# Kernel tuning notes

Measured on AMD Instinct MI355X. Metric: run time of the kernel, lower is better.

Reference implementation:

```python
import jax, jax.numpy as jnp
import numpy as np

ALPHA = 0.5  # leak rate (module default)


def setup_inputs() -> dict:
    key = jax.random.key(0)
    k1, k2, k3 = jax.random.split(key, 3)
    T, nInput, nRes = 4096, 4096, 2048
    x = jax.random.normal(k1, (T, nInput), dtype=jnp.float32)
    # gamma=0.01 scaled input weights, as in the module
    Win = 0.01 * jax.random.normal(k2, (nInput, nRes), dtype=jnp.float32)
    # recurrent weights ~ unit spectral radius (1/sqrt(N) scaling of iid gaussian)
    W = jax.random.normal(k3, (nRes, nRes), dtype=jnp.float32) / jnp.sqrt(nRes)
    return {"x": x, "Win": Win, "W": W}


def reference(x, Win, W):
    # Input projection is time-independent -> hoist out of the recurrence.
    uproj = x @ Win  # [T, nRes]

    def step(v, u):
        v_new = (1.0 - ALPHA) * v + ALPHA * jnp.tanh(v @ W + u)
        return v_new, v_new

    v0 = jnp.zeros((W.shape[0],), dtype=x.dtype)
    _, states = jax.lax.scan(step, v0, uproj)  # states: [T, nRes]
    return states
```

## Files before the change

### kernel.cpp

```cpp
#include <hip/hip_runtime.h>

#define NRES 2048
#define NBLK 256
#define RBUF 4

typedef unsigned long long u64;
typedef unsigned int u32;

__global__ __launch_bounds__(256) void transpose_k(const float* __restrict__ W,
                                                   float* __restrict__ Wt) {
  __shared__ float tile[32][33];
  const int tx = threadIdx.x, ty = threadIdx.y;
  const int x = blockIdx.x * 32 + tx;
  const int y0 = blockIdx.y * 32;
#pragma unroll
  for (int j = ty; j < 32; j += 8)
    tile[j][tx] = W[(size_t)(y0 + j) * NRES + x];
  __syncthreads();
  const int x2 = blockIdx.y * 32 + tx;
  const int y2 = blockIdx.x * 32;
#pragma unroll
  for (int j = ty; j < 32; j += 8)
    Wt[(size_t)(y2 + j) * NRES + x2] = tile[tx][j];
}

__global__ __launch_bounds__(256) void gemm_uproj(const float* __restrict__ X,
                                                  const float* __restrict__ B,
                                                  float* __restrict__ U,
                                                  int M, int N, int K) {
  __shared__ float As[16][128];
  __shared__ float Bs[16][128];
  const int tid = threadIdx.x;
  const int tx = tid & 15, ty = tid >> 4;
  const int m0 = blockIdx.y * 128, n0 = blockIdx.x * 128;

  float acc[8][8];
#pragma unroll
  for (int i = 0; i < 8; i++)
#pragma unroll
    for (int j = 0; j < 8; j++) acc[i][j] = 0.f;

  const int sam = tid >> 1, sak = (tid & 1) * 8;
  const int sbk = tid >> 4, sbn = (tid & 15) * 8;

  for (int k0 = 0; k0 < K; k0 += 16) {
    const float* ap = X + (size_t)(m0 + sam) * K + k0 + sak;
    float4 a0 = *(const float4*)(ap);
    float4 a1 = *(const float4*)(ap + 4);
    As[sak + 0][sam] = a0.x; As[sak + 1][sam] = a0.y;
    As[sak + 2][sam] = a0.z; As[sak + 3][sam] = a0.w;
    As[sak + 4][sam] = a1.x; As[sak + 5][sam] = a1.y;
    As[sak + 6][sam] = a1.z; As[sak + 7][sam] = a1.w;
    const float* bp = B + (size_t)(k0 + sbk) * N + n0 + sbn;
    *(float4*)&Bs[sbk][sbn]     = *(const float4*)(bp);
    *(float4*)&Bs[sbk][sbn + 4] = *(const float4*)(bp + 4);
    __syncthreads();
#pragma unroll
    for (int kk = 0; kk < 16; kk++) {
      float a[8], b[8];
      *(float4*)&a[0] = *(const float4*)&As[kk][ty * 8];
      *(float4*)&a[4] = *(const float4*)&As[kk][ty * 8 + 4];
      *(float4*)&b[0] = *(const float4*)&Bs[kk][tx * 8];
      *(float4*)&b[4] = *(const float4*)&Bs[kk][tx * 8 + 4];
#pragma unroll
      for (int i = 0; i < 8; i++)
#pragma unroll
        for (int j = 0; j < 8; j++) acc[i][j] += a[i] * b[j];
    }
    __syncthreads();
  }
#pragma unroll
  for (int i = 0; i < 8; i++) {
    float* dst = U + (size_t)(m0 + ty * 8 + i) * N + n0 + tx * 8;
    *(float4*)dst       = *(float4*)&acc[i][0];
    *(float4*)(dst + 4) = *(float4*)&acc[i][4];
  }
}

__global__ __launch_bounds__(256, 1) void esn_scan(const float* __restrict__ Wt,
                                                   const float* __restrict__ W,
                                                   u64* vtag,
                                                   float* __restrict__ UY,
                                                   int T) {
  __shared__ float v_lds[2][NRES];
  const int b = blockIdx.x;
  const int tid = threadIdx.x;
  const int wv = tid >> 6;
  const int lane = tid & 63;
  const int h = lane >> 5;
  const int s = lane & 31;
  const int j = b * 8 + wv * 2 + h;

  float2 w2[32];
  if (Wt) {
    const float2* wrow = (const float2*)(Wt + (size_t)j * NRES);
#pragma unroll
    for (int k = 0; k < 32; ++k) w2[k] = wrow[s + 32 * k];
  } else {
#pragma unroll
    for (int k = 0; k < 32; ++k) {
      w2[k].x = W[(size_t)(2 * s + 64 * k) * NRES + j];
      w2[k].y = W[(size_t)(2 * s + 64 * k + 1) * NRES + j];
    }
  }

  float vold = 0.f;
#pragma unroll
  for (int q = 0; q < 8; ++q) v_lds[0][tid + 256 * q] = 0.f;
  __syncthreads();

  for (int t = 0; t < T; ++t) {
    const int buf = t & 1;
    const size_t idx = (size_t)t * NRES + j;
    float u = (s == 0) ? UY[idx] : 0.f;

    if (t > 0) {
      u64* src = vtag + (size_t)((t - 1) & (RBUF - 1)) * NRES;
      unsigned done = 0;
      while (true) {
        u64 w[8];
#pragma unroll
        for (int q = 0; q < 8; ++q)
          if (!(done & (1u << q)))
            w[q] = __hip_atomic_load(&src[tid + 256 * q], __ATOMIC_RELAXED,
                                     __HIP_MEMORY_SCOPE_AGENT);
#pragma unroll
        for (int q = 0; q < 8; ++q) {
          if (!(done & (1u << q)) && (u32)(w[q] >> 32) == (u32)t) {
            v_lds[buf][tid + 256 * q] = __uint_as_float((u32)w[q]);
            done |= 1u << q;
          }
        }
        if (done == 0xFFu) break;
        __builtin_amdgcn_s_sleep(2);
      }
      __syncthreads();
    }

    float acc0 = 0.f, acc1 = 0.f;
#pragma unroll
    for (int k = 0; k < 32; k += 2) {
      float2 va = *(const float2*)&v_lds[buf][2 * s + 64 * k];
      float2 vb = *(const float2*)&v_lds[buf][2 * s + 64 * (k + 1)];
      acc0 += w2[k].x * va.x + w2[k].y * va.y;
      acc1 += w2[k + 1].x * vb.x + w2[k + 1].y * vb.y;
    }
    float acc = acc0 + acc1;
#pragma unroll
    for (int off = 16; off >= 1; off >>= 1) acc += __shfl_xor(acc, off);

    if (s == 0) {
      float xx = acc + u;
      float e = __expf(2.f * xx);
      float th = 1.f - 2.f / (e + 1.f);
      float vnew = 0.5f * vold + 0.5f * th;
      vold = vnew;
      UY[idx] = vnew;
      u64 w = ((u64)(u32)(t + 1) << 32) | (u64)__float_as_uint(vnew);
      (void)__hip_atomic_exchange(&vtag[(size_t)(t & (RBUF - 1)) * NRES + j],
                                  w, __ATOMIC_RELAXED,
                                  __HIP_MEMORY_SCOPE_AGENT);
    }
  }
}

extern "C" void kernel_launch(void* const* d_in, const int* in_sizes, int n_in,
                              void* d_out, int out_size, void* d_ws, size_t ws_size,
                              hipStream_t stream) {
  const float* x   = (const float*)d_in[0];
  const float* Win = (const float*)d_in[1];
  const float* W   = (const float*)d_in[2];
  float* U = (float*)d_out;

  const int T = out_size / NRES;
  const int K = in_sizes[0] / T;

  char* ws = (char*)d_ws;
  u64* vtag = (u64*)ws;
  const size_t vtag_bytes = (size_t)RBUF * NRES * sizeof(u64);
  float* Wt = nullptr;
  if (ws_size >= (1u << 20) + (size_t)NRES * NRES * sizeof(float))
    Wt = (float*)(ws + (1u << 20));

  hipMemsetAsync(vtag, 0, vtag_bytes, stream);

  if (Wt) transpose_k<<<dim3(NRES / 32, NRES / 32), dim3(32, 8), 0, stream>>>(W, Wt);

  gemm_uproj<<<dim3(NRES / 128, T / 128), 256, 0, stream>>>(x, Win, U, T, NRES, K);

  void* args[] = {(void*)&Wt, (void*)&W, (void*)&vtag, (void*)&U, (void*)&T};
  hipLaunchCooperativeKernel((const void*)esn_scan, dim3(NBLK), dim3(256), args,
                             0, stream);
}
```

Baseline: 14.55 ms.

## Use 64 blocks of 1024 threads for the ESN scan and drop poll sleep

Restructures the persistent recurrence kernel from 256 blocks of 256 threads to 64 blocks of 1024 threads. Each block now owns 32 reservoir units, and each thread polls two tagged state slots instead of eight. The s_sleep in the spin loop is removed. Fewer participating blocks means fewer agents polling the shared state buffer each step, but each block now has a larger intra-block barrier, only 64 CUs are used, and tighter polling adds memory traffic.

New measurement: 18.62 ms. +28.0%, slower.

```diff
diff --git a/kernel.cpp b/kernel.cpp
--- a/kernel.cpp
+++ b/kernel.cpp
@@ -1,7 +1,8 @@
 #include <hip/hip_runtime.h>
 
 #define NRES 2048
-#define NBLK 256
+#define NBLK 64
+#define NTHR 1024
 #define RBUF 4
 
 typedef unsigned long long u64;
@@ -77,11 +78,11 @@
   }
 }
 
-__global__ __launch_bounds__(256, 1) void esn_scan(const float* __restrict__ Wt,
-                                                   const float* __restrict__ W,
-                                                   u64* vtag,
-                                                   float* __restrict__ UY,
-                                                   int T) {
+__global__ __launch_bounds__(1024, 1) void esn_scan(const float* __restrict__ Wt,
+                                                    const float* __restrict__ W,
+                                                    u64* vtag,
+                                                    float* __restrict__ UY,
+                                                    int T) {
   __shared__ float v_lds[2][NRES];
   const int b = blockIdx.x;
   const int tid = threadIdx.x;
@@ -89,7 +90,7 @@
   const int lane = tid & 63;
   const int h = lane >> 5;
   const int s = lane & 31;
-  const int j = b * 8 + wv * 2 + h;
+  const int j = b * 32 + wv * 2 + h;
 
   float2 w2[32];
   if (Wt) {
@@ -105,8 +106,8 @@
   }
 
   float vold = 0.f;
-#pragma unroll
-  for (int q = 0; q < 8; ++q) v_lds[0][tid + 256 * q] = 0.f;
+  v_lds[0][tid] = 0.f;
+  v_lds[0][tid + NTHR] = 0.f;
   __syncthreads();
 
   for (int t = 0; t < T; ++t) {
@@ -117,22 +118,19 @@
     if (t > 0) {
       u64* src = vtag + (size_t)((t - 1) & (RBUF - 1)) * NRES;
       unsigned done = 0;
-      while (true) {
-        u64 w[8];
-#pragma unroll
-        for (int q = 0; q < 8; ++q)
-          if (!(done & (1u << q)))
-            w[q] = __hip_atomic_load(&src[tid + 256 * q], __ATOMIC_RELAXED,
-                                     __HIP_MEMORY_SCOPE_AGENT);
-#pragma unroll
-        for (int q = 0; q < 8; ++q) {
-          if (!(done & (1u << q)) && (u32)(w[q] >> 32) == (u32)t) {
-            v_lds[buf][tid + 256 * q] = __uint_as_float((u32)w[q]);
-            done |= 1u << q;
-          }
+      while (done != 3u) {
+        u64 w0 = __hip_atomic_load(&src[tid], __ATOMIC_RELAXED,
+                                   __HIP_MEMORY_SCOPE_AGENT);
+        u64 w1 = __hip_atomic_load(&src[tid + NTHR], __ATOMIC_RELAXED,
+                                   __HIP_MEMORY_SCOPE_AGENT);
+        if (!(done & 1u) && (u32)(w0 >> 32) == (u32)t) {
+          v_lds[buf][tid] = __uint_as_float((u32)w0);
+          done |= 1u;
         }
-        if (done == 0xFFu) break;
-        __builtin_amdgcn_s_sleep(2);
+        if (!(done & 2u) && (u32)(w1 >> 32) == (u32)t) {
+          v_lds[buf][tid + NTHR] = __uint_as_float((u32)w1);
+          done |= 2u;
+        }
       }
       __syncthreads();
     }
@@ -189,6 +187,6 @@
   gemm_uproj<<<dim3(NRES / 128, T / 128), 256, 0, stream>>>(x, Win, U, T, NRES, K);
 
   void* args[] = {(void*)&Wt, (void*)&W, (void*)&vtag, (void*)&U, (void*)&T};
-  hipLaunchCooperativeKernel((const void*)esn_scan, dim3(NBLK), dim3(256), args,
+  hipLaunchCooperativeKernel((const void*)esn_scan, dim3(NBLK), dim3(NTHR), args,
                              0, stream);
 }
```
